# Kernel tuning notes

Measured on AMD Instinct MI355X. Metric: run time of the kernel, lower is better.

The kernel has to match this reference:

```python
import jax, jax.numpy as jnp
import numpy as np

N_HEAD = 16
D_HEAD = 64
D_MODEL = 1024
SCALE = 1.0 / float(D_HEAD) ** 0.5
LN_EPS = 1e-5


def _rel_shift(x):
    # x: [b, n, i, j] -> Transformer-XL relative shift
    b, n, i, j = x.shape
    x = jnp.pad(x, ((0, 0), (0, 0), (0, 0), (1, 0)))  # zero-pad front of last dim
    x = x.reshape(b, n, j + 1, i)[:, :, 1:, :]
    return x.reshape(b, n, i, j)


def _layer_norm(x, g, b):
    mu = jnp.mean(x, axis=-1, keepdims=True)
    var = jnp.mean(jnp.square(x - mu), axis=-1, keepdims=True)
    return g * (x - mu) / jnp.sqrt(var + LN_EPS) + b


def setup_inputs() -> dict:
    key = jax.random.key(0)
    ks = jax.random.split(key, 8)
    qlen, bsz = 1024, 4
    w = jax.random.normal(ks[0], (qlen, bsz, D_MODEL), jnp.float32)
    r = jax.random.normal(ks[1], (qlen, D_MODEL), jnp.float32)
    r_w_bias = 0.02 * jax.random.normal(ks[2], (N_HEAD, D_HEAD), jnp.float32)
    r_r_bias = 0.02 * jax.random.normal(ks[3], (N_HEAD, D_HEAD), jnp.float32)
    attn_mask = jnp.triu(jnp.ones((qlen, qlen), bool), 1)  # causal, True = masked
    qkv_w = 0.02 * jax.random.normal(ks[4], (D_MODEL, 3 * N_HEAD * D_HEAD), jnp.float32)
    qkv_b = jnp.zeros((3 * N_HEAD * D_HEAD,), jnp.float32)
    rk_w = 0.02 * jax.random.normal(ks[5], (D_MODEL, N_HEAD * D_HEAD), jnp.float32)
    rk_b = jnp.zeros((N_HEAD * D_HEAD,), jnp.float32)
    o_w = 0.02 * jax.random.normal(ks[6], (N_HEAD * D_HEAD, D_MODEL), jnp.float32)
    o_b = jnp.zeros((D_MODEL,), jnp.float32)
    ln_g = jnp.ones((D_MODEL,), jnp.float32)
    ln_b = jnp.zeros((D_MODEL,), jnp.float32)
    return {"w": w, "r": r, "r_w_bias": r_w_bias, "r_r_bias": r_r_bias,
            "qkv_w": qkv_w, "qkv_b": qkv_b, "rk_w": rk_w, "rk_b": rk_b,
            "o_w": o_w, "o_b": o_b, "ln_g": ln_g, "ln_b": ln_b,
            "attn_mask": attn_mask}


def reference(w, r, r_w_bias, r_r_bias, qkv_w, qkv_b, rk_w, rk_b, o_w, o_b, ln_g, ln_b, attn_mask):
    qlen, bsz, _ = w.shape
    # post-lnorm path (pre_lnorm=False)
    heads = w @ qkv_w + qkv_b                       # [q, b, 3*H*D]
    q, k, v = jnp.split(heads, 3, axis=-1)
    q = q.reshape(qlen, bsz, N_HEAD, D_HEAD)
    k = k.reshape(qlen, bsz, N_HEAD, D_HEAD)
    v = v.reshape(qlen, bsz, N_HEAD, D_HEAD)
    rk = (r @ rk_w + rk_b).reshape(-1, N_HEAD, D_HEAD)  # [rlen, H, D]
    AC = jnp.einsum('ibnd,jbnd->bnij', q + r_w_bias, k)
    BD = _rel_shift(jnp.einsum('ibnd,jnd->bnij', q + r_r_bias, rk))
    score = SCALE * (AC + BD)                       # [b, H, q, k]
    score = jnp.where(attn_mask[None, None, :, :], -jnp.inf, score)
    prob = jax.nn.softmax(score, axis=-1)
    vec = jnp.einsum('bnij,jbnd->ibnd', prob, v).reshape(qlen, bsz, N_HEAD * D_HEAD)
    attn_out = vec @ o_w + o_b
    return _layer_norm(w + attn_out, ln_g, ln_b)
```

## Files before the change

kernel.cpp:

```cpp
#include <hip/hip_runtime.h>
#include <math.h>

#define QL 1024
#define BSZ 4
#define NH 16
#define DH 64
#define DM 1024
#define SCALE_F 0.125f

typedef __attribute__((ext_vector_type(8))) short bf16x8;
typedef __attribute__((ext_vector_type(4))) float f32x4;

__device__ __forceinline__ unsigned short f2bf(float f) {
  union { float f; unsigned int u; } c; c.f = f;
  unsigned int u = c.u;
  u += 0x7FFFu + ((u >> 16) & 1u);
  return (unsigned short)(u >> 16);
}
__device__ __forceinline__ float bf2f(unsigned short u) {
  union { unsigned int i; float f; } c; c.i = ((unsigned int)u) << 16;
  return c.f;
}
__device__ __forceinline__ float2 bfp2f(const unsigned short* p) {
  unsigned int u = *(const unsigned int*)p;
  union { unsigned int u; float f; } lo, hi;
  lo.u = (u & 0xFFFFu) << 16;
  hi.u = u & 0xFFFF0000u;
  return make_float2(lo.f, hi.f);
}

__device__ __forceinline__ void ld_lds16(const unsigned short* g, unsigned short* l) {
  __builtin_amdgcn_global_load_lds(
      (const __attribute__((address_space(1))) unsigned int*)g,
      (__attribute__((address_space(3))) unsigned int*)l, 16, 0, 0);
}

__device__ __forceinline__ bf16x8 frag64(const unsigned short* lds, int n, int s) {
  return *(const bf16x8*)(lds + n * 64 + ((s ^ (n & 7)) * 8));
}

template <int CTRL>
__device__ __forceinline__ float dpp_mv(float x) {
  return __int_as_float(__builtin_amdgcn_update_dpp(
      0, __float_as_int(x), CTRL, 0xf, 0xf, true));
}
__device__ __forceinline__ float rowsum16(float x) {
  x += dpp_mv<0x121>(x);
  x += dpp_mv<0x122>(x);
  x += dpp_mv<0x124>(x);
  x += dpp_mv<0x128>(x);
  return x;
}

__global__ __launch_bounds__(256) void prep_kernel(
    const float* __restrict__ w, const float* __restrict__ r,
    const float* __restrict__ qkv_w, const float* __restrict__ rk_w,
    const float* __restrict__ o_w,
    unsigned short* __restrict__ wb, unsigned short* __restrict__ rb,
    unsigned short* __restrict__ qkv_wt, unsigned short* __restrict__ rk_wt,
    unsigned short* __restrict__ o_wt, float* __restrict__ drk) {
  __shared__ __align__(16) unsigned short t[64][72];
  const int bid = blockIdx.x, tid = threadIdx.x;
  if (bid >= 3840) {
    int idx = (bid - 3840) * 256 + tid;
    ((float4*)drk)[idx] = make_float4(0.f, 0.f, 0.f, 0.f);
    return;
  }
  if (bid < 2560) {
    const float* in = (bid < 2048) ? w : r;
    unsigned short* out = (bid < 2048) ? wb : rb;
    int idx = ((bid < 2048) ? bid : (bid - 2048)) * 256 + tid;
    float4 a = *(const float4*)(in + (size_t)idx * 8);
    float4 b = *(const float4*)(in + (size_t)idx * 8 + 4);
    unsigned short o[8] = {f2bf(a.x), f2bf(a.y), f2bf(a.z), f2bf(a.w),
                           f2bf(b.x), f2bf(b.y), f2bf(b.z), f2bf(b.w)};
    *(uint4*)(out + (size_t)idx * 8) = *(const uint4*)o;
    return;
  }
  const float* in; unsigned short* out; int N, n0, k0;
  if (bid < 3328) {
    int l = bid - 2560; in = qkv_w; out = qkv_wt; N = 3072;
    n0 = (l % 48) * 64; k0 = (l / 48) * 64;
  } else if (bid < 3584) {
    int l = bid - 3328; in = rk_w; out = rk_wt; N = 1024;
    n0 = (l & 15) * 64; k0 = (l >> 4) * 64;
  } else {
    int l = bid - 3584; in = o_w; out = o_wt; N = 1024;
    n0 = (l & 15) * 64; k0 = (l >> 4) * 64;
  }
  for (int f = tid; f < 1024; f += 256) {
    int rr = f >> 4, c4 = (f & 15) * 4;
    float4 v = *(const float4*)(in + (size_t)(k0 + rr) * N + n0 + c4);
    t[c4 + 0][rr] = f2bf(v.x); t[c4 + 1][rr] = f2bf(v.y);
    t[c4 + 2][rr] = f2bf(v.z); t[c4 + 3][rr] = f2bf(v.w);
  }
  __syncthreads();
  for (int f = tid; f < 512; f += 256) {
    int rr = f >> 3, seg = (f & 7) * 8;
    *(uint4*)(out + (size_t)(n0 + rr) * 1024 + k0 + seg) = *(const uint4*)&t[rr][seg];
  }
}

__global__ __launch_bounds__(512) void gemm12(
    const unsigned short* __restrict__ wb, const unsigned short* __restrict__ rb,
    const unsigned short* __restrict__ qkv_wt, const unsigned short* __restrict__ rk_wt,
    const float* __restrict__ qkv_b, const float* __restrict__ rk_b,
    const float* __restrict__ rwb, const float* __restrict__ rrb,
    unsigned short* __restrict__ qbf, unsigned short* __restrict__ kbf,
    unsigned short* __restrict__ vtb, unsigned short* __restrict__ rkbf,
    float* __restrict__ drk) {
  __shared__ __align__(16) unsigned short As[2 * 4096];
  __shared__ __align__(16) unsigned short Bs[2 * 4096];
  const int bid = blockIdx.x, tid = threadIdx.x;
  const int w = tid >> 6, lane = tid & 63;
  const int quad = lane >> 4, l15 = lane & 15;
  const int wr = w >> 2, wc = w & 3;
  const bool job0 = bid < 768;
  const unsigned short *A, *BT;
  const float* bias;
  int bm, bn;
  if (job0) {
    A = wb; BT = qkv_wt; bias = qkv_b;
    bn = (bid % 24) * 128; bm = (bid / 24) * 128;
  } else {
    int l = bid - 768;
    A = rb; BT = rk_wt; bias = rk_b;
    bn = (l & 7) * 128; bm = (l >> 3) * 128;
  }
  const int srow = w * 16 + (lane >> 2);
  const int sseg = (lane & 3) ^ ((lane >> 2) & 3);
  f32x4 acc[4][2] = {};

  auto stage = [&](int bf, int k0) {
    ld_lds16(A + (size_t)(bm + srow) * 1024 + k0 + sseg * 8, As + bf * 4096 + w * 512);
    ld_lds16(BT + (size_t)(bn + srow) * 1024 + k0 + sseg * 8, Bs + bf * 4096 + w * 512);
  };

  int buf = 0;
  stage(0, 0);
  for (int k0 = 0; k0 < 1024; k0 += 32) {
    __syncthreads();
    if (k0 + 32 < 1024) stage(buf ^ 1, k0 + 32);
    const unsigned short* Al = As + buf * 4096;
    const unsigned short* Bl = Bs + buf * 4096;
    const int sa = quad ^ (l15 & 3);
    bf16x8 af[4], bfr[2];
#pragma unroll
    for (int rt = 0; rt < 4; ++rt)
      af[rt] = *(const bf16x8*)&Al[(wr * 64 + rt * 16 + l15) * 32 + sa * 8];
#pragma unroll
    for (int nt = 0; nt < 2; ++nt)
      bfr[nt] = *(const bf16x8*)&Bl[(wc * 32 + nt * 16 + l15) * 32 + sa * 8];
#pragma unroll
    for (int rt = 0; rt < 4; ++rt)
#pragma unroll
      for (int nt = 0; nt < 2; ++nt)
        acc[rt][nt] = __builtin_amdgcn_mfma_f32_16x16x32_bf16(af[rt], bfr[nt], acc[rt][nt], 0, 0, 0);
    buf ^= 1;
  }

  if (job0) {
#pragma unroll
    for (int rt = 0; rt < 4; ++rt)
#pragma unroll
      for (int nt = 0; nt < 2; ++nt) {
        int gc = bn + wc * 32 + nt * 16 + l15;
        float bv = bias[gc];
        int part = gc >> 10, h = (gc >> 6) & 15, d = gc & 63;
#pragma unroll
        for (int reg = 0; reg < 4; ++reg) {
          int gr = bm + wr * 64 + rt * 16 + quad * 4 + reg;
          float val = acc[rt][nt][reg] + bv;
          int i = gr >> 2, b = gr & 3;
          if (part == 0)
            qbf[((size_t)((b * NH + h) * QL + i)) * DH + d] = f2bf(val);
          else if (part == 1)
            kbf[((size_t)((b * NH + h) * QL + i)) * DH + d] = f2bf(val);
          else
            vtb[((size_t)((b * NH + h) * DH + d)) * QL + i] = f2bf(val);
        }
      }
  } else {
    const int h = (bn + wc * 32) >> 6;
    float df[2];
#pragma unroll
    for (int nt = 0; nt < 2; ++nt) {
      int dd = (wc & 1) * 32 + nt * 16 + l15;
      df[nt] = rrb[h * DH + dd] - rwb[h * DH + dd];
    }
#pragma unroll
    for (int rt = 0; rt < 4; ++rt) {
      float s[4] = {0.f, 0.f, 0.f, 0.f};
#pragma unroll
      for (int nt = 0; nt < 2; ++nt) {
        int gc = bn + wc * 32 + nt * 16 + l15;
        float bv = bias[gc];
        int d = gc & 63;
#pragma unroll
        for (int reg = 0; reg < 4; ++reg) {
          int gr = bm + wr * 64 + rt * 16 + quad * 4 + reg;
          float val = acc[rt][nt][reg] + bv;
          rkbf[((size_t)(h * QL + gr)) * DH + d] = f2bf(val);
          s[reg] += val * df[nt];
        }
      }
#pragma unroll
      for (int reg = 0; reg < 4; ++reg) {
        float v = s[reg];
        v += __shfl_xor(v, 1);
        v += __shfl_xor(v, 2);
        v += __shfl_xor(v, 4);
        v += __shfl_xor(v, 8);
        if (l15 == 0) {
          int j = bm + wr * 64 + rt * 16 + quad * 4 + reg;
          atomicAdd(&drk[h * QL + j], v);
        }
      }
    }
  }
}

__global__ __launch_bounds__(512) void gemm_o(
    const unsigned short* __restrict__ A, const unsigned short* __restrict__ BT,
    const float* __restrict__ bias, float* __restrict__ Cf) {
  __shared__ __align__(16) unsigned short As[2 * 4096];
  __shared__ __align__(16) unsigned short Bs[2 * 2048];
  const int tid = threadIdx.x;
  const int w = tid >> 6, lane = tid & 63;
  const int quad = lane >> 4, l15 = lane & 15;
  const int wr = w >> 1, wc = w & 1;
  const int bm = blockIdx.y * 128, bn = blockIdx.x * 64;
  const int srow = w * 16 + (lane >> 2);
  const int sseg = (lane & 3) ^ ((lane >> 2) & 3);
  f32x4 acc[2][2] = {};

  auto stage = [&](int bf, int k0) {
    ld_lds16(A + (size_t)(bm + srow) * 1024 + k0 + sseg * 8, As + bf * 4096 + w * 512);
    if (w < 4)
      ld_lds16(BT + (size_t)(bn + srow) * 1024 + k0 + sseg * 8, Bs + bf * 2048 + w * 512);
  };

  int buf = 0;
  stage(0, 0);
  for (int k0 = 0; k0 < 1024; k0 += 32) {
    __syncthreads();
    if (k0 + 32 < 1024) stage(buf ^ 1, k0 + 32);
    const unsigned short* Al = As + buf * 4096;
    const unsigned short* Bl = Bs + buf * 2048;
    const int sa = quad ^ (l15 & 3);
    bf16x8 af[2], bfr[2];
#pragma unroll
    for (int rt = 0; rt < 2; ++rt)
      af[rt] = *(const bf16x8*)&Al[(wr * 32 + rt * 16 + l15) * 32 + sa * 8];
#pragma unroll
    for (int nt = 0; nt < 2; ++nt)
      bfr[nt] = *(const bf16x8*)&Bl[(wc * 32 + nt * 16 + l15) * 32 + sa * 8];
#pragma unroll
    for (int rt = 0; rt < 2; ++rt)
#pragma unroll
      for (int nt = 0; nt < 2; ++nt)
        acc[rt][nt] = __builtin_amdgcn_mfma_f32_16x16x32_bf16(af[rt], bfr[nt], acc[rt][nt], 0, 0, 0);
    buf ^= 1;
  }

#pragma unroll
  for (int rt = 0; rt < 2; ++rt)
#pragma unroll
    for (int nt = 0; nt < 2; ++nt) {
      int gc = bn + wc * 32 + nt * 16 + l15;
      float bv = bias[gc];
#pragma unroll
      for (int reg = 0; reg < 4; ++reg) {
        int gr = bm + wr * 32 + rt * 16 + quad * 4 + reg;
        Cf[(size_t)gr * DM + gc] = acc[rt][nt][reg] + bv;
      }
    }
}

__global__ __launch_bounds__(512, 4) void attn_kernel(
    const unsigned short* __restrict__ qbf, const unsigned short* __restrict__ kbf,
    const unsigned short* __restrict__ vtb, const unsigned short* __restrict__ rkb,
    const float* __restrict__ drk, const float* __restrict__ rwb,
    unsigned short* __restrict__ vecb) {
  __shared__ __align__(16) unsigned short SH[40960];
  unsigned short* Ks = SH;
  unsigned short* Vs = SH + 16384;
  unsigned short* PM = SH + 32768;

  const int tid = threadIdx.x;
  const int w = tid >> 6, lane = tid & 63;
  const int g = w >> 2, wg = w & 3;
  const int quad = lane >> 4, l15 = lane & 15;
  const int bh = blockIdx.x, b = bh >> 4, h = bh & 15;
  const int yA = blockIdx.y;

  const unsigned short* kB0 = kbf + (size_t)bh * QL * DH;
  const unsigned short* vB0 = vtb + (size_t)bh * DH * QL;
  const unsigned short* rB0 = rkb + (size_t)h * QL * DH;
  const float* drkh = drk + h * QL;
  unsigned short* pmw = PM + w * 1024;
  float* ml = (float*)(PM + 4096);

  const int srow8 = lane >> 3, sseg8 = lane & 7;

  for (int stream = 0; stream < 2; ++stream) {
    const int y = (stream == 0) ? (15 - yA) : yA;
    const int i0 = y * 64, tS = y, T = tS + 1;
    const int nR = (T + 1) >> 1;
    const int myBase = g ? nR : 0;
    const int myN = g ? (T - nR) : nR;

    bf16x8 qf[2];
    {
      int qrow = i0 + wg * 16 + l15;
      const unsigned short* qp = qbf + ((size_t)bh * QL + qrow) * DH;
#pragma unroll
      for (int s = 0; s < 2; ++s) {
        int off = s * 32 + quad * 8;
        uint4 raw = *(const uint4*)(qp + off);
        const unsigned short* ru = (const unsigned short*)&raw;
        float4 wb0 = *(const float4*)(rwb + h * DH + off);
        float4 wb1 = *(const float4*)(rwb + h * DH + off + 4);
        union { bf16x8 v; unsigned short u[8]; } qc;
        qc.u[0] = f2bf(bf2f(ru[0]) + wb0.x); qc.u[1] = f2bf(bf2f(ru[1]) + wb0.y);
        qc.u[2] = f2bf(bf2f(ru[2]) + wb0.z); qc.u[3] = f2bf(bf2f(ru[3]) + wb0.w);
        qc.u[4] = f2bf(bf2f(ru[4]) + wb1.x); qc.u[5] = f2bf(bf2f(ru[5]) + wb1.y);
        qc.u[6] = f2bf(bf2f(ru[6]) + wb1.z); qc.u[7] = f2bf(bf2f(ru[7]) + wb1.w);
        qf[s] = qc.v;
      }
    }

    float lrow[4] = {0.f, 0.f, 0.f, 0.f};
    f32x4 pv[4];
#pragma unroll
    for (int r = 0; r < 4; ++r) pv[r] = (f32x4){0.f, 0.f, 0.f, 0.f};

    auto stage_mine = [&](int p, int buf) {
      int tt = min(myBase + p, tS);
      const unsigned short* kb = kB0 + (size_t)(tt * 64) * DH;
      const unsigned short* vb = vB0 + tt * 64;
      unsigned short* kd = Ks + buf * 8192 + g * 4096;
      unsigned short* vd = Vs + buf * 8192 + g * 4096;
#pragma unroll
      for (int ii = 0; ii < 2; ++ii) {
        int row = wg * 16 + ii * 8 + srow8;
        int gs = sseg8 ^ (row & 7);
        ld_lds16(kb + (size_t)row * DH + gs * 8, kd + (wg * 16 + ii * 8) * 64);
        ld_lds16(vb + (size_t)row * QL + gs * 8, vd + (wg * 16 + ii * 8) * 64);
      }
    };

    auto rel_frag = [&](int gb, f32x4& c) {
      int row = min(gb + l15, QL - 1);
      const unsigned short* rp = rB0 + (size_t)row * DH;
      f32x4 a = {0.f, 0.f, 0.f, 0.f};
      a = __builtin_amdgcn_mfma_f32_16x16x32_bf16(qf[0], *(const bf16x8*)(rp + quad * 8), a, 0, 0, 0);
      a = __builtin_amdgcn_mfma_f32_16x16x32_bf16(qf[1], *(const bf16x8*)(rp + 32 + quad * 8), a, 0, 0, 0);
      float dv = drkh[row];
      a[0] += dv; a[1] += dv; a[2] += dv; a[3] += dv;
      c = a;
    };

    f32x4 rc[5];
    {
      const int Bt0 = 1008 - i0 + 64 * myBase - 16 * wg;
#pragma unroll
      for (int f = 0; f < 5; ++f) rel_frag(Bt0 + 16 * f, rc[f]);
    }

    stage_mine(0, 0);
    for (int p = 0; p < nR; ++p) {
      __syncthreads();
      if (p + 1 < nR) stage_mine(p + 1, (p + 1) & 1);
      if (p < myN) {
        const int t = myBase + p;
        const bool diag = (t == tS);
        const unsigned short* ksl = Ks + (p & 1) * 8192 + g * 4096;
        const unsigned short* vsl = Vs + (p & 1) * 8192 + g * 4096;

        if (p > 0) {
          rc[0] = rc[4];
          const int Bt = 1008 - i0 + 64 * t - 16 * wg;
#pragma unroll
          for (int f = 1; f < 5; ++f) rel_frag(Bt + 16 * f, rc[f]);
        }

        f32x4 sacc[4];
#pragma unroll
        for (int nt = 0; nt < 4; ++nt) {
          int n = nt * 16 + l15;
          f32x4 c = {0.f, 0.f, 0.f, 0.f};
          c = __builtin_amdgcn_mfma_f32_16x16x32_bf16(qf[0], frag64(ksl, n, quad), c, 0, 0, 0);
          c = __builtin_amdgcn_mfma_f32_16x16x32_bf16(qf[1], frag64(ksl, n, 4 + quad), c, 0, 0, 0);
          sacc[nt] = c;
        }

#pragma unroll
        for (int r = 0; r < 4; ++r) {
          const int il = wg * 16 + quad * 4 + r;
          const int ls = l15 + 15 - quad * 4 - r;
          const int srcl = (quad << 4) | (ls & 15);
          float rot[5];
#pragma unroll
          for (int f = 0; f < 5; ++f) rot[f] = __shfl(rc[f][r], srcl, 64);
          const bool lo = ls < 16;
          float psum = 0.f;
          const int prow = quad * 4 + r;
          const int psw = prow & 7;
#pragma unroll
          for (int nt = 0; nt < 4; ++nt) {
            float band = lo ? rot[nt] : rot[nt + 1];
            float s = (sacc[nt][r] + band) * SCALE_F;
            if (diag && (nt * 16 + l15) > il) s = -1e30f;
            float e = __expf(s);
            psum += e;
            int jl = nt * 16 + l15;
            pmw[prow * 64 + (((jl >> 3) ^ psw) << 3) + (jl & 7)] = f2bf(e);
          }
          lrow[r] += rowsum16(psum);
        }

        bf16x8 pf0 = frag64(pmw, l15, quad);
        bf16x8 pf1 = frag64(pmw, l15, 4 + quad);
#pragma unroll
        for (int nt = 0; nt < 4; ++nt) {
          int n = nt * 16 + l15;
          pv[nt] = __builtin_amdgcn_mfma_f32_16x16x32_bf16(pf0, frag64(vsl, n, quad), pv[nt], 0, 0, 0);
          pv[nt] = __builtin_amdgcn_mfma_f32_16x16x32_bf16(pf1, frag64(vsl, n, 4 + quad), pv[nt], 0, 0, 0);
        }
      }
    }

    __syncthreads();
    if (g == 1) {
#pragma unroll
      for (int r = 0; r < 4; ++r) {
        int il = wg * 16 + quad * 4 + r;
#pragma unroll
        for (int nt = 0; nt < 4; ++nt)
          PM[il * 64 + nt * 16 + l15] = f2bf(pv[nt][r]);
        if (l15 == 0) ml[il] = lrow[r];
      }
    }
    __syncthreads();
    if (g == 0) {
#pragma unroll
      for (int r = 0; r < 4; ++r) {
        int il = wg * 16 + quad * 4 + r;
        float inv = 1.0f / (lrow[r] + ml[il]);
#pragma unroll
        for (int nt = 0; nt < 4; ++nt) {
          float pv1 = bf2f(PM[il * 64 + nt * 16 + l15]);
          float val = (pv[nt][r] + pv1) * inv;
          vecb[((size_t)((i0 + il) * BSZ + b)) * DM + h * DH + nt * 16 + l15] = f2bf(val);
        }
      }
    }
  }
}

__global__ __launch_bounds__(256) void ln_kernel(
    const float* __restrict__ w, const float* __restrict__ attn,
    const float* __restrict__ g, const float* __restrict__ bta,
    float* __restrict__ out) {
  __shared__ float red[4];
  __shared__ float sval[2];
  const int row = blockIdx.x, tid = threadIdx.x;
  const float* wr = w + (size_t)row * DM;
  const float* ar = attn + (size_t)row * DM;
  float4 wv = *(const float4*)(wr + tid * 4);
  float4 av = *(const float4*)(ar + tid * 4);
  float x0 = wv.x + av.x, x1 = wv.y + av.y, x2 = wv.z + av.z, x3 = wv.w + av.w;
  float s = x0 + x1 + x2 + x3;
#pragma unroll
  for (int off = 32; off; off >>= 1) s += __shfl_down(s, off, 64);
  const int lane = tid & 63, wvi = tid >> 6;
  if (lane == 0) red[wvi] = s;
  __syncthreads();
  if (tid == 0) sval[0] = (red[0] + red[1] + red[2] + red[3]) * (1.0f / 1024.0f);
  __syncthreads();
  const float mu = sval[0];
  float d0 = x0 - mu, d1 = x1 - mu, d2 = x2 - mu, d3 = x3 - mu;
  float vs2 = d0 * d0 + d1 * d1 + d2 * d2 + d3 * d3;
#pragma unroll
  for (int off = 32; off; off >>= 1) vs2 += __shfl_down(vs2, off, 64);
  if (lane == 0) red[wvi] = vs2;
  __syncthreads();
  if (tid == 0)
    sval[1] = rsqrtf((red[0] + red[1] + red[2] + red[3]) * (1.0f / 1024.0f) + 1e-5f);
  __syncthreads();
  const float inv = sval[1];
  float4 gv = *(const float4*)(g + tid * 4);
  float4 bv = *(const float4*)(bta + tid * 4);
  float4 ov;
  ov.x = gv.x * d0 * inv + bv.x;
  ov.y = gv.y * d1 * inv + bv.y;
  ov.z = gv.z * d2 * inv + bv.z;
  ov.w = gv.w * d3 * inv + bv.w;
  *(float4*)(out + (size_t)row * DM + tid * 4) = ov;
}

extern "C" void kernel_launch(void* const* d_in, const int* in_sizes, int n_in,
                              void* d_out, int out_size, void* d_ws, size_t ws_size,
                              hipStream_t stream) {
  const float* w     = (const float*)d_in[0];
  const float* r     = (const float*)d_in[1];
  const float* rwb   = (const float*)d_in[2];
  const float* rrb   = (const float*)d_in[3];
  const float* qkv_w = (const float*)d_in[4];
  const float* qkv_b = (const float*)d_in[5];
  const float* rk_w  = (const float*)d_in[6];
  const float* rk_b  = (const float*)d_in[7];
  const float* o_w   = (const float*)d_in[8];
  const float* o_b   = (const float*)d_in[9];
  const float* ln_g  = (const float*)d_in[10];
  const float* ln_b  = (const float*)d_in[11];

  float* out = (float*)d_out;
  char* p = (char*)d_ws;
  unsigned short* wb     = (unsigned short*)p; p += (size_t)4096 * 1024 * 2;
  unsigned short* rb     = (unsigned short*)p; p += (size_t)1024 * 1024 * 2;
  unsigned short* qkv_wt = (unsigned short*)p; p += (size_t)3072 * 1024 * 2;
  unsigned short* rk_wt  = (unsigned short*)p; p += (size_t)1024 * 1024 * 2;
  unsigned short* o_wt   = (unsigned short*)p; p += (size_t)1024 * 1024 * 2;
  unsigned short* qbf    = (unsigned short*)p; p += (size_t)BSZ * NH * QL * DH * 2;
  unsigned short* kbf    = (unsigned short*)p; p += (size_t)BSZ * NH * QL * DH * 2;
  unsigned short* vtb    = (unsigned short*)p; p += (size_t)BSZ * NH * QL * DH * 2;
  unsigned short* rkbf   = (unsigned short*)p; p += (size_t)NH * QL * DH * 2;
  float*          drk    = (float*)p;          p += (size_t)NH * QL * 4;
  unsigned short* vecb   = (unsigned short*)p; p += (size_t)4096 * 1024 * 2;
  float*          attnf  = (float*)p;          p += (size_t)4096 * 1024 * 4;

  prep_kernel<<<3856, 256, 0, stream>>>(w, r, qkv_w, rk_w, o_w,
                                        wb, rb, qkv_wt, rk_wt, o_wt, drk);
  gemm12<<<832, 512, 0, stream>>>(wb, rb, qkv_wt, rk_wt, qkv_b, rk_b, rwb, rrb,
                                  qbf, kbf, vtb, rkbf, drk);
  attn_kernel<<<dim3(64, 8), 512, 0, stream>>>(qbf, kbf, vtb, rkbf, drk, rwb, vecb);
  gemm_o<<<dim3(16, 32), 512, 0, stream>>>(vecb, o_wt, o_b, attnf);
  ln_kernel<<<4096, 256, 0, stream>>>(w, attnf, ln_g, ln_b, out);
}
```

Baseline: 290.0 us.

## Simplify attention to one query tile per 256-thread block without KV split

The attention kernel drops the two-stream pairing of a heavy and a light query tile and the split of the KV range across two 4-wave groups. Each block now owns one 64-row query tile and walks all causal KV tiles itself with 4 waves, launching 1024 blocks of 256 threads. This removes the cross-group merge through LDS and its extra barriers, and halves the shared-memory footprint so more blocks can be resident. It trades away load balancing within a block: blocks handle anywhere from 1 to 16 tiles, and each wave has a longer serial KV loop. The relative-position fragments for the next tile are now computed after the PV MFMAs.

```diff
diff --git a/kernel.cpp b/kernel.cpp
--- a/kernel.cpp
+++ b/kernel.cpp
@@ -20,13 +20,6 @@
 __device__ __forceinline__ float bf2f(unsigned short u) {
   union { unsigned int i; float f; } c; c.i = ((unsigned int)u) << 16;
   return c.f;
-}
-__device__ __forceinline__ float2 bfp2f(const unsigned short* p) {
-  unsigned int u = *(const unsigned int*)p;
-  union { unsigned int u; float f; } lo, hi;
-  lo.u = (u & 0xFFFFu) << 16;
-  hi.u = u & 0xFFFF0000u;
-  return make_float2(lo.f, hi.f);
 }
 
 __device__ __forceinline__ void ld_lds16(const unsigned short* g, unsigned short* l) {
@@ -277,186 +270,158 @@
     }
 }
 
-__global__ __launch_bounds__(512, 4) void attn_kernel(
+__global__ __launch_bounds__(256, 4) void attn_kernel(
     const unsigned short* __restrict__ qbf, const unsigned short* __restrict__ kbf,
     const unsigned short* __restrict__ vtb, const unsigned short* __restrict__ rkb,
     const float* __restrict__ drk, const float* __restrict__ rwb,
     unsigned short* __restrict__ vecb) {
-  __shared__ __align__(16) unsigned short SH[40960];
+  __shared__ __align__(16) unsigned short SH[20480];
   unsigned short* Ks = SH;
-  unsigned short* Vs = SH + 16384;
-  unsigned short* PM = SH + 32768;
+  unsigned short* Vs = SH + 8192;
+  unsigned short* PM = SH + 16384;
 
   const int tid = threadIdx.x;
-  const int w = tid >> 6, lane = tid & 63;
-  const int g = w >> 2, wg = w & 3;
+  const int wg = tid >> 6, lane = tid & 63;
   const int quad = lane >> 4, l15 = lane & 15;
   const int bh = blockIdx.x, b = bh >> 4, h = bh & 15;
-  const int yA = blockIdx.y;
+  const int y = 15 - (int)blockIdx.y;
+  const int i0 = y * 64, tS = y, T = y + 1;
 
   const unsigned short* kB0 = kbf + (size_t)bh * QL * DH;
   const unsigned short* vB0 = vtb + (size_t)bh * DH * QL;
   const unsigned short* rB0 = rkb + (size_t)h * QL * DH;
   const float* drkh = drk + h * QL;
-  unsigned short* pmw = PM + w * 1024;
-  float* ml = (float*)(PM + 4096);
+  unsigned short* pmw = PM + wg * 1024;
 
   const int srow8 = lane >> 3, sseg8 = lane & 7;
 
-  for (int stream = 0; stream < 2; ++stream) {
-    const int y = (stream == 0) ? (15 - yA) : yA;
-    const int i0 = y * 64, tS = y, T = tS + 1;
-    const int nR = (T + 1) >> 1;
-    const int myBase = g ? nR : 0;
-    const int myN = g ? (T - nR) : nR;
-
-    bf16x8 qf[2];
-    {
-      int qrow = i0 + wg * 16 + l15;
-      const unsigned short* qp = qbf + ((size_t)bh * QL + qrow) * DH;
-#pragma unroll
-      for (int s = 0; s < 2; ++s) {
-        int off = s * 32 + quad * 8;
-        uint4 raw = *(const uint4*)(qp + off);
-        const unsigned short* ru = (const unsigned short*)&raw;
-        float4 wb0 = *(const float4*)(rwb + h * DH + off);
-        float4 wb1 = *(const float4*)(rwb + h * DH + off + 4);
-        union { bf16x8 v; unsigned short u[8]; } qc;
-        qc.u[0] = f2bf(bf2f(ru[0]) + wb0.x); qc.u[1] = f2bf(bf2f(ru[1]) + wb0.y);
-        qc.u[2] = f2bf(bf2f(ru[2]) + wb0.z); qc.u[3] = f2bf(bf2f(ru[3]) + wb0.w);
-        qc.u[4] = f2bf(bf2f(ru[4]) + wb1.x); qc.u[5] = f2bf(bf2f(ru[5]) + wb1.y);
-        qc.u[6] = f2bf(bf2f(ru[6]) + wb1.z); qc.u[7] = f2bf(bf2f(ru[7]) + wb1.w);
-        qf[s] = qc.v;
+  bf16x8 qf[2];
+  {
+    int qrow = i0 + wg * 16 + l15;
+    const unsigned short* qp = qbf + ((size_t)bh * QL + qrow) * DH;
+#pragma unroll
+    for (int s = 0; s < 2; ++s) {
+      int off = s * 32 + quad * 8;
+      uint4 raw = *(const uint4*)(qp + off);
+      const unsigned short* ru = (const unsigned short*)&raw;
+      float4 wb0 = *(const float4*)(rwb + h * DH + off);
+      float4 wb1 = *(const float4*)(rwb + h * DH + off + 4);
+      union { bf16x8 v; unsigned short u[8]; } qc;
+      qc.u[0] = f2bf(bf2f(ru[0]) + wb0.x); qc.u[1] = f2bf(bf2f(ru[1]) + wb0.y);
+      qc.u[2] = f2bf(bf2f(ru[2]) + wb0.z); qc.u[3] = f2bf(bf2f(ru[3]) + wb0.w);
+      qc.u[4] = f2bf(bf2f(ru[4]) + wb1.x); qc.u[5] = f2bf(bf2f(ru[5]) + wb1.y);
+      qc.u[6] = f2bf(bf2f(ru[6]) + wb1.z); qc.u[7] = f2bf(bf2f(ru[7]) + wb1.w);
+      qf[s] = qc.v;
+    }
+  }
+
+  auto rel_frag = [&](int gb, f32x4& c) {
+    int row = min(gb + l15, QL - 1);
+    const unsigned short* rp = rB0 + (size_t)row * DH;
+    f32x4 a = {0.f, 0.f, 0.f, 0.f};
+    a = __builtin_amdgcn_mfma_f32_16x16x32_bf16(qf[0], *(const bf16x8*)(rp + quad * 8), a, 0, 0, 0);
+    a = __builtin_amdgcn_mfma_f32_16x16x32_bf16(qf[1], *(const bf16x8*)(rp + 32 + quad * 8), a, 0, 0, 0);
+    float dv = drkh[row];
+    a[0] += dv; a[1] += dv; a[2] += dv; a[3] += dv;
+    c = a;
+  };
+
+  auto stage_tile = [&](int t, int buf) {
+    const unsigned short* kb = kB0 + (size_t)(t * 64) * DH;
+    const unsigned short* vb = vB0 + t * 64;
+    unsigned short* kd = Ks + buf * 4096;
+    unsigned short* vd = Vs + buf * 4096;
+#pragma unroll
+    for (int ii = 0; ii < 2; ++ii) {
+      int row = wg * 16 + ii * 8 + srow8;
+      int gs = sseg8 ^ (row & 7);
+      ld_lds16(kb + (size_t)row * DH + gs * 8, kd + (wg * 16 + ii * 8) * 64);
+      ld_lds16(vb + (size_t)row * QL + gs * 8, vd + (wg * 16 + ii * 8) * 64);
+    }
+  };
+
+  float lrow[4] = {0.f, 0.f, 0.f, 0.f};
+  f32x4 pv[4];
+#pragma unroll
+  for (int r = 0; r < 4; ++r) pv[r] = (f32x4){0.f, 0.f, 0.f, 0.f};
+
+  f32x4 rc[5];
+  {
+    const int Bt0 = 1008 - i0 - 16 * wg;
+#pragma unroll
+    for (int f = 0; f < 5; ++f) rel_frag(Bt0 + 16 * f, rc[f]);
+  }
+
+  int buf = 0;
+  stage_tile(0, 0);
+  for (int t = 0; t < T; ++t) {
+    __syncthreads();
+    if (t + 1 < T) stage_tile(t + 1, buf ^ 1);
+    const bool diag = (t == tS);
+    const unsigned short* ksl = Ks + buf * 4096;
+    const unsigned short* vsl = Vs + buf * 4096;
+
+    f32x4 sacc[4];
+#pragma unroll
+    for (int nt = 0; nt < 4; ++nt) {
+      int n = nt * 16 + l15;
+      f32x4 c = {0.f, 0.f, 0.f, 0.f};
+      c = __builtin_amdgcn_mfma_f32_16x16x32_bf16(qf[0], frag64(ksl, n, quad), c, 0, 0, 0);
+      c = __builtin_amdgcn_mfma_f32_16x16x32_bf16(qf[1], frag64(ksl, n, 4 + quad), c, 0, 0, 0);
+      sacc[nt] = c;
+    }
+
+#pragma unroll
+    for (int r = 0; r < 4; ++r) {
+      const int il = wg * 16 + quad * 4 + r;
+      const int ls = l15 + 15 - quad * 4 - r;
+      const int srcl = (quad << 4) | (ls & 15);
+      float rot[5];
+#pragma unroll
+      for (int f = 0; f < 5; ++f) rot[f] = __shfl(rc[f][r], srcl, 64);
+      const bool lo = ls < 16;
+      float psum = 0.f;
+      const int prow = quad * 4 + r;
+      const int psw = prow & 7;
+#pragma unroll
+      for (int nt = 0; nt < 4; ++nt) {
+        float band = lo ? rot[nt] : rot[nt + 1];
+        float s = (sacc[nt][r] + band) * SCALE_F;
+        if (diag && (nt * 16 + l15) > il) s = -1e30f;
+        float e = __expf(s);
+        psum += e;
+        int jl = nt * 16 + l15;
+        pmw[prow * 64 + (((jl >> 3) ^ psw) << 3) + (jl & 7)] = f2bf(e);
       }
-    }
-
-    float lrow[4] = {0.f, 0.f, 0.f, 0.f};
-    f32x4 pv[4];
-#pragma unroll
-    for (int r = 0; r < 4; ++r) pv[r] = (f32x4){0.f, 0.f, 0.f, 0.f};
-
-    auto stage_mine = [&](int p, int buf) {
-      int tt = min(myBase + p, tS);
-      const unsigned short* kb = kB0 + (size_t)(tt * 64) * DH;
-      const unsigned short* vb = vB0 + tt * 64;
-      unsigned short* kd = Ks + buf * 8192 + g * 4096;
-      unsigned short* vd = Vs + buf * 8192 + g * 4096;
-#pragma unroll
-      for (int ii = 0; ii < 2; ++ii) {
-        int row = wg * 16 + ii * 8 + srow8;
-        int gs = sseg8 ^ (row & 7);
-        ld_lds16(kb + (size_t)row * DH + gs * 8, kd + (wg * 16 + ii * 8) * 64);
-        ld_lds16(vb + (size_t)row * QL + gs * 8, vd + (wg * 16 + ii * 8) * 64);
-      }
-    };
-
-    auto rel_frag = [&](int gb, f32x4& c) {
-      int row = min(gb + l15, QL - 1);
-      const unsigned short* rp = rB0 + (size_t)row * DH;
-      f32x4 a = {0.f, 0.f, 0.f, 0.f};
-      a = __builtin_amdgcn_mfma_f32_16x16x32_bf16(qf[0], *(const bf16x8*)(rp + quad * 8), a, 0, 0, 0);
-      a = __builtin_amdgcn_mfma_f32_16x16x32_bf16(qf[1], *(const bf16x8*)(rp + 32 + quad * 8), a, 0, 0, 0);
-      float dv = drkh[row];
-      a[0] += dv; a[1] += dv; a[2] += dv; a[3] += dv;
-      c = a;
-    };
-
-    f32x4 rc[5];
-    {
-      const int Bt0 = 1008 - i0 + 64 * myBase - 16 * wg;
-#pragma unroll
-      for (int f = 0; f < 5; ++f) rel_frag(Bt0 + 16 * f, rc[f]);
-    }
-
-    stage_mine(0, 0);
-    for (int p = 0; p < nR; ++p) {
-      __syncthreads();
-      if (p + 1 < nR) stage_mine(p + 1, (p + 1) & 1);
-      if (p < myN) {
-        const int t = myBase + p;
-        const bool diag = (t == tS);
-        const unsigned short* ksl = Ks + (p & 1) * 8192 + g * 4096;
-        const unsigned short* vsl = Vs + (p & 1) * 8192 + g * 4096;
-
-        if (p > 0) {
-          rc[0] = rc[4];
-          const int Bt = 1008 - i0 + 64 * t - 16 * wg;
-#pragma unroll
-          for (int f = 1; f < 5; ++f) rel_frag(Bt + 16 * f, rc[f]);
-        }
-
-        f32x4 sacc[4];
-#pragma unroll
-        for (int nt = 0; nt < 4; ++nt) {
-          int n = nt * 16 + l15;
-          f32x4 c = {0.f, 0.f, 0.f, 0.f};
-          c = __builtin_amdgcn_mfma_f32_16x16x32_bf16(qf[0], frag64(ksl, n, quad), c, 0, 0, 0);
-          c = __builtin_amdgcn_mfma_f32_16x16x32_bf16(qf[1], frag64(ksl, n, 4 + quad), c, 0, 0, 0);
-          sacc[nt] = c;
-        }
-
-#pragma unroll
-        for (int r = 0; r < 4; ++r) {
-          const int il = wg * 16 + quad * 4 + r;
-          const int ls = l15 + 15 - quad * 4 - r;
-          const int srcl = (quad << 4) | (ls & 15);
-          float rot[5];
-#pragma unroll
-          for (int f = 0; f < 5; ++f) rot[f] = __shfl(rc[f][r], srcl, 64);
-          const bool lo = ls < 16;
-          float psum = 0.f;
-          const int prow = quad * 4 + r;
-          const int psw = prow & 7;
-#pragma unroll
-          for (int nt = 0; nt < 4; ++nt) {
-            float band = lo ? rot[nt] : rot[nt + 1];
-            float s = (sacc[nt][r] + band) * SCALE_F;
-            if (diag && (nt * 16 + l15) > il) s = -1e30f;
-            float e = __expf(s);
-            psum += e;
-            int jl = nt * 16 + l15;
-            pmw[prow * 64 + (((jl >> 3) ^ psw) << 3) + (jl & 7)] = f2bf(e);
-          }
-          lrow[r] += rowsum16(psum);
-        }
-
-        bf16x8 pf0 = frag64(pmw, l15, quad);
-        bf16x8 pf1 = frag64(pmw, l15, 4 + quad);
-#pragma unroll
-        for (int nt = 0; nt < 4; ++nt) {
-          int n = nt * 16 + l15;
-          pv[nt] = __builtin_amdgcn_mfma_f32_16x16x32_bf16(pf0, frag64(vsl, n, quad), pv[nt], 0, 0, 0);
-          pv[nt] = __builtin_amdgcn_mfma_f32_16x16x32_bf16(pf1, frag64(vsl, n, 4 + quad), pv[nt], 0, 0, 0);
-        }
-      }
-    }
-
-    __syncthreads();
-    if (g == 1) {
-#pragma unroll
-      for (int r = 0; r < 4; ++r) {
-        int il = wg * 16 + quad * 4 + r;
-#pragma unroll
-        for (int nt = 0; nt < 4; ++nt)
-          PM[il * 64 + nt * 16 + l15] = f2bf(pv[nt][r]);
-        if (l15 == 0) ml[il] = lrow[r];
-      }
-    }
-    __syncthreads();
-    if (g == 0) {
-#pragma unroll
-      for (int r = 0; r < 4; ++r) {
-        int il = wg * 16 + quad * 4 + r;
-        float inv = 1.0f / (lrow[r] + ml[il]);
-#pragma unroll
-        for (int nt = 0; nt < 4; ++nt) {
-          float pv1 = bf2f(PM[il * 64 + nt * 16 + l15]);
-          float val = (pv[nt][r] + pv1) * inv;
-          vecb[((size_t)((i0 + il) * BSZ + b)) * DM + h * DH + nt * 16 + l15] = f2bf(val);
-        }
-      }
-    }
-  }
+      lrow[r] += rowsum16(psum);
+    }
+
+    bf16x8 pf0 = frag64(pmw, l15, quad);
+    bf16x8 pf1 = frag64(pmw, l15, 4 + quad);
+#pragma unroll
+    for (int nt = 0; nt < 4; ++nt) {
+      int n = nt * 16 + l15;
+      pv[nt] = __builtin_amdgcn_mfma_f32_16x16x32_bf16(pf0, frag64(vsl, n, quad), pv[nt], 0, 0, 0);
+      pv[nt] = __builtin_amdgcn_mfma_f32_16x16x32_bf16(pf1, frag64(vsl, n, 4 + quad), pv[nt], 0, 0, 0);
+    }
+
+    if (t + 1 < T) {
+      rc[0] = rc[4];
+      const int Bt = 1008 - i0 + 64 * (t + 1) - 16 * wg;
+#pragma unroll
+      for (int f = 1; f < 5; ++f) rel_frag(Bt + 16 * f, rc[f]);
+    }
+    buf ^= 1;
+  }
+
+#pragma unroll
+  for (int nt = 0; nt < 4; ++nt)
+#pragma unroll
+    for (int r = 0; r < 4; ++r) {
+      int il = wg * 16 + quad * 4 + r;
+      float val = pv[nt][r] / lrow[r];
+      vecb[((size_t)((i0 + il) * BSZ + b)) * DM + h * DH + nt * 16 + l15] = f2bf(val);
+    }
 }
 
 __global__ __launch_bounds__(256) void ln_kernel(
@@ -535,7 +500,7 @@
                                         wb, rb, qkv_wt, rk_wt, o_wt, drk);
   gemm12<<<832, 512, 0, stream>>>(wb, rb, qkv_wt, rk_wt, qkv_b, rk_b, rwb, rrb,
                                   qbf, kbf, vtb, rkbf, drk);
-  attn_kernel<<<dim3(64, 8), 512, 0, stream>>>(qbf, kbf, vtb, rkbf, drk, rwb, vecb);
+  attn_kernel<<<dim3(64, 16), 256, 0, stream>>>(qbf, kbf, vtb, rkbf, drk, rwb, vecb);
   gemm_o<<<dim3(16, 32), 512, 0, stream>>>(vecb, o_wt, o_b, attnf);
   ln_kernel<<<4096, 256, 0, stream>>>(w, attnf, ln_g, ln_b, out);
 }
```

Result: faster. 280.9 us (-3.1%).
